# Optimization experiments

Measured on AMD Instinct MI355X. Metric: run time of the kernel, lower is better.

The kernel has to match this reference:

```python
import jax, jax.numpy as jnp
import numpy as np
from jax import lax

D_MODEL = 512
D_INNER = 1024   # expand=2
D_STATE = 16
D_CONV = 4
DT_RANK = 32     # ceil(d_model/16)
D_FFN = 2048
EPS = 1e-6


def _layernorm(x, g, b):
    mu = jnp.mean(x, axis=-1, keepdims=True)
    var = jnp.mean((x - mu) ** 2, axis=-1, keepdims=True)
    return (x - mu) * lax.rsqrt(var + EPS) * g + b


def _mamba(x, in_w, conv_w, conv_b, xproj_w, dt_w, dt_b, A_log, D_vec, out_w):
    # x: [B, L, d_model]
    B, L, _ = x.shape
    xz = jnp.einsum('bld,ed->ble', x, in_w)           # [B, L, 2*d_inner]
    xc, z = xz[..., :D_INNER], xz[..., D_INNER:]
    # causal depthwise conv over time
    xt = xc.transpose(0, 2, 1)                        # [B, d_inner, L]
    kern = conv_w[:, None, :]                         # [d_inner, 1, d_conv]
    xt = lax.conv_general_dilated(xt, kern, (1,), [(D_CONV - 1, 0)],
                                  feature_group_count=D_INNER)
    xc = jax.nn.silu(xt.transpose(0, 2, 1) + conv_b)  # [B, L, d_inner]
    # input-dependent SSM parameters
    x_dbl = jnp.einsum('bld,ed->ble', xc, xproj_w)    # [B, L, dt_rank+2*d_state]
    dt = x_dbl[..., :DT_RANK]
    Bm = x_dbl[..., DT_RANK:DT_RANK + D_STATE]
    Cm = x_dbl[..., DT_RANK + D_STATE:]
    delta = jax.nn.softplus(jnp.einsum('blr,dr->bld', dt, dt_w) + dt_b)  # [B, L, d_inner]
    A = -jnp.exp(A_log)                               # [d_inner, d_state]

    def step(h, inp):
        d_t, u_t, b_t, c_t = inp                      # [B,di],[B,di],[B,ds],[B,ds]
        dA = jnp.exp(d_t[:, :, None] * A)             # [B, di, ds]
        dBu = (d_t * u_t)[:, :, None] * b_t[:, None, :]
        h = dA * h + dBu
        y = jnp.einsum('bds,bs->bd', h, c_t)
        return h, y

    h0 = jnp.zeros((B, D_INNER, D_STATE), x.dtype)
    xs = (delta.transpose(1, 0, 2), xc.transpose(1, 0, 2),
          Bm.transpose(1, 0, 2), Cm.transpose(1, 0, 2))
    _, ys = lax.scan(step, h0, xs)                    # [L, B, d_inner]
    y = ys.transpose(1, 0, 2) + xc * D_vec
    y = y * jax.nn.silu(z)
    return jnp.einsum('ble,de->bld', y, out_w)        # [B, L, d_model]


def setup_inputs() -> dict:
    key = jax.random.key(0)
    ks = iter(jax.random.split(key, 40))
    B, S, T = 8, 512, 1024

    def nrm(shape, scale=0.02):
        return jax.random.normal(next(ks), shape, dtype=jnp.float32) * scale

    def mamba_params(prefix):
        A_log = jnp.log(jnp.broadcast_to(jnp.arange(1, D_STATE + 1, dtype=jnp.float32),
                                         (D_INNER, D_STATE)))
        return {
            prefix + '_in_w': nrm((2 * D_INNER, D_MODEL)),
            prefix + '_conv_w': nrm((D_INNER, D_CONV), 0.1),
            prefix + '_conv_b': jnp.zeros((D_INNER,), jnp.float32),
            prefix + '_xproj_w': nrm((DT_RANK + 2 * D_STATE, D_INNER)),
            prefix + '_dt_w': nrm((D_INNER, DT_RANK), 0.1),
            prefix + '_dt_b': jnp.full((D_INNER,), -4.0, jnp.float32),
            prefix + '_A_log': A_log,
            prefix + '_D_vec': jnp.ones((D_INNER,), jnp.float32),
            prefix + '_out_w': nrm((D_MODEL, D_INNER)),
        }

    inp = {
        'tgt': jax.random.normal(next(ks), (B, S, D_MODEL), dtype=jnp.float32),
        'memory': jax.random.normal(next(ks), (B, T, D_MODEL), dtype=jnp.float32),
    }
    inp.update(mamba_params('self'))
    inp.update(mamba_params('cross'))
    inp.update({
        'ln1_g': jnp.ones((D_MODEL,), jnp.float32), 'ln1_b': jnp.zeros((D_MODEL,), jnp.float32),
        'ln2_g': jnp.ones((D_MODEL,), jnp.float32), 'ln2_b': jnp.zeros((D_MODEL,), jnp.float32),
        'ln3_g': jnp.ones((D_MODEL,), jnp.float32), 'ln3_b': jnp.zeros((D_MODEL,), jnp.float32),
        'ffn_w1': nrm((D_FFN, D_MODEL)), 'ffn_b1': jnp.zeros((D_FFN,), jnp.float32),
        'ffn_w2': nrm((D_MODEL, D_FFN)), 'ffn_b2': jnp.zeros((D_MODEL,), jnp.float32),
    })
    return inp


def reference(tgt, memory,
              self_in_w, self_conv_w, self_conv_b, self_xproj_w, self_dt_w, self_dt_b,
              self_A_log, self_D_vec, self_out_w,
              cross_in_w, cross_conv_w, cross_conv_b, cross_xproj_w, cross_dt_w, cross_dt_b,
              cross_A_log, cross_D_vec, cross_out_w,
              ln1_g, ln1_b, ln2_g, ln2_b, ln3_g, ln3_b,
              ffn_w1, ffn_b1, ffn_w2, ffn_b2):
    S = tgt.shape[1]
    # self-Mamba block (post-norm, dropout=0)
    t2 = _mamba(tgt, self_in_w, self_conv_w, self_conv_b, self_xproj_w,
                self_dt_w, self_dt_b, self_A_log, self_D_vec, self_out_w)
    t = _layernorm(tgt + t2, ln1_g, ln1_b)
    # cross-Mamba: scan over [memory; tgt], keep last S steps
    cat = jnp.concatenate([memory, t], axis=1)
    c2 = _mamba(cat, cross_in_w, cross_conv_w, cross_conv_b, cross_xproj_w,
                cross_dt_w, cross_dt_b, cross_A_log, cross_D_vec, cross_out_w)[:, -S:]
    t = _layernorm(t + c2, ln2_g, ln2_b)
    # positionwise FFN
    f = jnp.einsum('bld,fd->blf', t, ffn_w1) + ffn_b1
    f = jax.nn.relu(f)
    f = jnp.einsum('blf,df->bld', f, ffn_w2) + ffn_b2
    t = _layernorm(t + f, ln3_g, ln3_b)
    return t
```

## Files before the change

kernel.cpp:

```cpp
#include <hip/hip_runtime.h>
#include <math.h>

#define DM    512
#define DI    1024
#define DSN   16
#define DTR   32
#define DFFN  2048
#define BB    8
#define SS    512
#define TTM   1024
#define LCAT  1536
#define CONV_R 8

#define ACT_NONE     0
#define ACT_RELU     1
#define ACT_DELTA    3
#define ACT_XDBL     4

typedef __attribute__((ext_vector_type(8))) short short8;
typedef __attribute__((ext_vector_type(8))) unsigned short ushort8;
typedef __attribute__((ext_vector_type(4))) float f32x4;

#define L2E 1.4426950408889634f

__device__ __forceinline__ unsigned short f2b(float f) {
    unsigned int u = __float_as_uint(f);
    return (unsigned short)((u + 0x7FFFu + ((u >> 16) & 1u)) >> 16);
}
__device__ __forceinline__ float b2f(unsigned short h) {
    return __uint_as_float(((unsigned int)h) << 16);
}
__device__ __forceinline__ float fast_softplus(float v) {
    return (v > 20.f) ? v : __logf(1.f + __expf(v));
}
__device__ __forceinline__ float fexp2(float x) {
#if __has_builtin(__builtin_amdgcn_exp2f)
    return __builtin_amdgcn_exp2f(x);
#else
    float r; asm("v_exp_f32 %0, %1" : "=v"(r) : "v"(x)); return r;
#endif
}
__device__ __forceinline__ float frcp(float x) {
    return __builtin_amdgcn_rcpf(x);
}
__device__ __forceinline__ void gld16(const void* g, void* l) {
    __builtin_amdgcn_global_load_lds(
        (const __attribute__((address_space(1))) void*)g,
        (__attribute__((address_space(3))) void*)l, 16, 0, 0);
}

__device__ __forceinline__ int map_row(int m, int mb, int bs, int ro) {
    int q = m / mb;
    return q * bs + ro + (m - q * mb);
}

__global__ __launch_bounds__(256) void mgemm_kernel(
    const unsigned short* __restrict__ A, int mb, int bs, int ro,
    const unsigned short* __restrict__ W, const float* __restrict__ bias,
    float* __restrict__ Cf, unsigned short* __restrict__ Cb,
    float* __restrict__ C2, float* __restrict__ Cf2,
    int N, int K, int act,
    int omb, int obs, int oro, int ldc, int nofs, int pstr,
    int ysplit, int amb2, int abs2, int aro2, int wofs2,
    int omb2, int obs2, int oro2, int nofs2)
{
    __shared__ __align__(16) unsigned short As[128 * 64];
    __shared__ __align__(16) unsigned short Bs[128 * 64];
    int tid = threadIdx.x;
    int lane = tid & 63, wave = tid >> 6;
    int wy = wave >> 1, wx = wave & 1;
    int bx = blockIdx.x, by = blockIdx.y;
    int nx = gridDim.x, ny = gridDim.y;
    const unsigned short* Wp = W;
    if (ysplit) {
        if (by >= ysplit) {
            by -= ysplit; ny = gridDim.y - ysplit;
            mb = amb2; bs = abs2; ro = aro2; Wp += wofs2;
            omb = omb2; obs = obs2; oro = oro2; nofs = nofs2;
        } else ny = ysplit;
    }
    int f = by * nx + bx;
    int xcd = f & 7, j2 = f >> 3;
    int bandh = ny >> 3;
    int m0 = (xcd * bandh + j2 / nx) * 128;
    int n0 = (j2 % nx) * 128;
    int Kh = K / gridDim.z;
    int kbeg = blockIdx.z * Kh, kend = kbeg + Kh;
    float* Cfo = Cf;
    const float* biaso = bias;
    if (blockIdx.z) { Cfo = Cf2 + (size_t)(blockIdx.z - 1) * pstr; biaso = nullptr; }

    unsigned aoff[4], boff[4];
    unsigned short* la[4];
    unsigned short* lb[4];
    #pragma unroll
    for (int j = 0; j < 4; j++) {
        int c  = wave * 256 + j * 64 + lane;
        int r  = c >> 3;
        int q  = c & 7;
        int g  = q ^ (r & 7);
        int arow = map_row(m0 + r, mb, bs, ro);
        aoff[j] = (unsigned)(arow * K + g * 8);
        boff[j] = (unsigned)((n0 + r) * K + g * 8);
        la[j] = As + (size_t)(wave * 256 + j * 64) * 8;
        lb[j] = Bs + (size_t)(wave * 256 + j * 64) * 8;
    }
    int fm = lane & 15, fg = lane >> 4;
    int sw = fg ^ (fm & 3);
    int b2 = (fm >> 2) & 1;
    const unsigned short* arp = As + ((size_t)(wy * 64 + fm) * 8 + sw) * 8;
    const unsigned short* brp = Bs + ((size_t)(wx * 64 + fm) * 8 + sw) * 8;

    f32x4 acc[4][4];
    #pragma unroll
    for (int i = 0; i < 4; i++)
        #pragma unroll
        for (int j = 0; j < 4; j++) acc[i][j] = 0.f;

    for (int k0 = kbeg; k0 < kend; k0 += 64) {
        #pragma unroll
        for (int j = 0; j < 4; j++) {
            gld16(A  + aoff[j] + k0, la[j]);
            gld16(Wp + boff[j] + k0, lb[j]);
        }
        __syncthreads();
        #pragma unroll
        for (int h = 0; h < 2; h++) {
            int ho = ((h ^ b2) * 32);
            short8 af[4], bfr[4];
            #pragma unroll
            for (int t = 0; t < 4; t++) af[t]  = *(const short8*)(arp + ho + t * 1024);
            #pragma unroll
            for (int t = 0; t < 4; t++) bfr[t] = *(const short8*)(brp + ho + t * 1024);
            #pragma unroll
            for (int i = 0; i < 4; i++)
                #pragma unroll
                for (int j = 0; j < 4; j++)
                    acc[i][j] = __builtin_amdgcn_mfma_f32_16x16x32_bf16(af[i], bfr[j], acc[i][j], 0, 0, 0);
        }
        __syncthreads();
    }

    int en = lane & 15, em = (lane >> 4) * 4;
    if (act == ACT_XDBL) {
        size_t zb = (size_t)blockIdx.z * omb;
        #pragma unroll
        for (int j = 0; j < 4; j++) {
            int n = n0 + wx * 64 + j * 16 + en;
            if (n >= 64) continue;
            #pragma unroll
            for (int i = 0; i < 4; i++) {
                int mbase = m0 + wy * 64 + i * 16 + em;
                #pragma unroll
                for (int r = 0; r < 4; r++)
                    C2[(zb + mbase + r) * 64 + n] = acc[i][j][r];
            }
        }
        return;
    }
    if (act == ACT_DELTA) {
        #pragma unroll
        for (int j = 0; j < 4; j++) {
            int n = n0 + wx * 64 + j * 16 + en;
            float bv = bias[n];
            #pragma unroll
            for (int i = 0; i < 4; i++) {
                int mbase = m0 + wy * 64 + i * 16 + em;
                #pragma unroll
                for (int r = 0; r < 4; r++) {
                    float v = acc[i][j][r] + bv;
                    Cb[(size_t)(mbase + r) * 1024 + n] = f2b(fast_softplus(v));
                }
            }
        }
        return;
    }
    #pragma unroll
    for (int j = 0; j < 4; j++) {
        int n = n0 + wx * 64 + j * 16 + en;
        float bv = biaso ? biaso[n] : 0.f;
        #pragma unroll
        for (int i = 0; i < 4; i++) {
            int mbase = m0 + wy * 64 + i * 16 + em;
            #pragma unroll
            for (int r = 0; r < 4; r++) {
                float v = acc[i][j][r] + bv;
                if (act == ACT_RELU) v = v > 0.f ? v : 0.f;
                int orow = map_row(mbase + r, omb, obs, oro);
                size_t off = (size_t)orow * ldc + nofs + n;
                if (Cb) Cb[off] = f2b(v);
                else    Cfo[off] = v;
            }
        }
    }
}

__global__ __launch_bounds__(256) void xdbl_combine(
    const float* __restrict__ pxd, unsigned short* __restrict__ dtb,
    float* __restrict__ bcout, int M, int Z)
{
    int idx = blockIdx.x * 256 + threadIdx.x;
    int m = idx >> 4, n4 = idx & 15;
    int n = n4 * 4;
    float4 s = make_float4(0.f, 0.f, 0.f, 0.f);
    for (int z = 0; z < Z; z++) {
        float4 p = *(const float4*)(pxd + ((size_t)z * M + m) * 64 + n);
        s.x += p.x; s.y += p.y; s.z += p.z; s.w += p.w;
    }
    if (n < 32) {
        ((ushort4*)(dtb + (size_t)m * 64))[n4] =
            make_ushort4(f2b(s.x), f2b(s.y), f2b(s.z), f2b(s.w));
    } else {
        *(float4*)(bcout + (size_t)m * 32 + (n - 32)) = s;
        ((ushort4*)(dtb + (size_t)m * 64))[n4] = make_ushort4(0, 0, 0, 0);
    }
}

struct PrepPtrs {
    const float* tgt; const float* mem;
    const float* w[6];
    const float* xpj_s; const float* xpj_c;
    const float* dtw_s; const float* dtw_c;
    unsigned short* tgtb; unsigned short* catb; unsigned short* wb;
    unsigned short* xprojb_s; unsigned short* xprojb_c;
    unsigned short* dtwb_s; unsigned short* dtwb_c;
};
__global__ __launch_bounds__(256) void prep_kernel(PrepPtrs p)
{
    int u = blockIdx.x * 256 + threadIdx.x;
    if (u < 524288) {
        float4 v = ((const float4*)p.tgt)[u];
        ((ushort4*)p.tgtb)[u] = make_ushort4(f2b(v.x), f2b(v.y), f2b(v.z), f2b(v.w));
        return;
    }
    if (u < 1572864) {
        int f = u - 524288;
        int b = f >> 17, rem = f & 131071;
        float4 v = ((const float4*)p.mem)[f];
        ((ushort4*)p.catb)[(size_t)b * 196608 + rem] =
            make_ushort4(f2b(v.x), f2b(v.y), f2b(v.z), f2b(v.w));
        return;
    }
    if (u < 2883584) {
        const int cum[7] = {0, 262144, 524288, 655360, 786432, 1048576, 1310720};
        int i = u - 1572864;
        int seg = 0;
        #pragma unroll
        for (int s = 1; s < 6; s++) seg += (i >= cum[s]);
        float4 v = ((const float4*)p.w[seg])[i - cum[seg]];
        ((ushort4*)p.wb)[i] = make_ushort4(f2b(v.x), f2b(v.y), f2b(v.z), f2b(v.w));
        return;
    }
    if (u < 2949120) {
        int i = u - 2883584;
        const float* src = p.xpj_s;
        unsigned short* dst = p.xprojb_s;
        if (i >= 32768) { i -= 32768; src = p.xpj_c; dst = p.xprojb_c; }
        int n = i >> 8;
        ushort4 o = make_ushort4(0, 0, 0, 0);
        if (n < 64) {
            float4 v = ((const float4*)src)[i];
            o = make_ushort4(f2b(v.x), f2b(v.y), f2b(v.z), f2b(v.w));
        }
        ((ushort4*)dst)[i] = o;
        return;
    }
    {
        int i = u - 2949120;
        const float* src = p.dtw_s;
        unsigned short* dst = p.dtwb_s;
        if (i >= 16384) { i -= 16384; src = p.dtw_c; dst = p.dtwb_c; }
        int n = i >> 4, c = (i & 15) * 4;
        ushort4 o = make_ushort4(0, 0, 0, 0);
        if (c < 32) {
            float4 v = *(const float4*)(src + n * 32 + c);
            o = make_ushort4(f2b(v.x), f2b(v.y), f2b(v.z), f2b(v.w));
        }
        ((ushort4*)dst)[i] = o;
    }
}

__global__ __launch_bounds__(256) void conv_silu_kernel(
    const unsigned short* __restrict__ xz,
    const float* __restrict__ cw,
    const float* __restrict__ cb,
    unsigned short* __restrict__ xc, int L, int total)
{
    int idx = blockIdx.x * blockDim.x + threadIdx.x;
    if (idx >= total) return;
    int d8 = idx & 127;
    int d0 = d8 * 8;
    int t  = idx >> 7;
    int nq = L / CONV_R;
    int b  = t / nq;
    int l0 = (t - b * nq) * CONV_R;
    size_t rbase = (size_t)b * L + l0;

    float4 wv[8];
    #pragma unroll
    for (int j = 0; j < 8; j++) wv[j] = *(const float4*)(cw + (d0 + j) * 4);
    float bias[8];
    {
        float4 c0 = ((const float4*)(cb + d0))[0];
        float4 c1 = ((const float4*)(cb + d0))[1];
        bias[0]=c0.x; bias[1]=c0.y; bias[2]=c0.z; bias[3]=c0.w;
        bias[4]=c1.x; bias[5]=c1.y; bias[6]=c1.z; bias[7]=c1.w;
    }
    ushort8 win[CONV_R + 3];
    #pragma unroll
    for (int k = 0; k < 3; k++) {
        ushort8 z;
        #pragma unroll
        for (int j = 0; j < 8; j++) z[j] = 0;
        win[k] = (l0 - 3 + k >= 0)
            ? *(const ushort8*)(xz + (rbase - 3 + k) * 2048 + d0) : z;
    }
    #pragma unroll
    for (int i = 0; i < CONV_R; i++)
        win[3 + i] = *(const ushort8*)(xz + (rbase + i) * 2048 + d0);

    const float* w = (const float*)&wv[0];
    #pragma unroll
    for (int i = 0; i < CONV_R; i++) {
        float acc[8];
        #pragma unroll
        for (int j = 0; j < 8; j++) acc[j] = bias[j];
        #pragma unroll
        for (int k = 0; k < 4; k++) {
            ushort8 v = win[i + k];
            #pragma unroll
            for (int j = 0; j < 8; j++)
                acc[j] = fmaf(b2f(v[j]), w[j * 4 + k], acc[j]);
        }
        ushort8 o;
        #pragma unroll
        for (int j = 0; j < 8; j++)
            o[j] = f2b(acc[j] * frcp(1.f + __expf(-acc[j])));
        *(ushort8*)(xc + (rbase + i) * 1024 + d0) = o;
    }
}

__global__ __launch_bounds__(256) void scan_part1(
    const unsigned short* __restrict__ delta, const unsigned short* __restrict__ xc,
    const float* __restrict__ bc, const float* __restrict__ A_log,
    float* __restrict__ part_h, float* __restrict__ part_s, int L, int CH, int NCr)
{
    __shared__ float bcs[24 * 16];
    int tid = threadIdx.x;
    int dblk = blockIdx.x & 3;
    int rest = blockIdx.x >> 2;
    int c    = rest % NCr;
    int b    = rest / NCr;
    if (c == NCr - 1) return;
    int l0 = c * CH;
    for (int i = tid; i < CH * 16; i += 256) {
        int lr = i >> 4, s = i & 15;
        bcs[i] = bc[((size_t)b * L + l0 + lr) * 32 + s];
    }
    __syncthreads();
    int d    = dblk * 256 + tid;
    float A2[DSN];
    {
        const float4* ap = (const float4*)(A_log + d * DSN);
        #pragma unroll
        for (int q = 0; q < 4; q++) {
            float4 a4 = ap[q];
            A2[q*4+0] = -__expf(a4.x) * L2E;
            A2[q*4+1] = -__expf(a4.y) * L2E;
            A2[q*4+2] = -__expf(a4.z) * L2E;
            A2[q*4+3] = -__expf(a4.w) * L2E;
        }
    }
    float h[DSN];
    #pragma unroll
    for (int s = 0; s < DSN; s++) h[s] = 0.f;
    float ssum = 0.f;
    size_t rb = (size_t)b * L + l0;
    float dl = b2f(delta[rb * DI + d]);
    float u  = b2f(xc[rb * DI + d]);
    for (int i = 0; i < CH; i++) {
        float cdl = dl, cu = u;
        if (i + 1 < CH) {
            size_t rn = rb + i + 1;
            dl = b2f(delta[rn * DI + d]);
            u  = b2f(xc[rn * DI + d]);
        }
        const float* Bm = bcs + i * 16;
        float du = cdl * cu;
        ssum += cdl;
        #pragma unroll
        for (int s = 0; s < DSN; s++)
            h[s] = fmaf(fexp2(cdl * A2[s]), h[s], du * Bm[s]);
    }
    size_t base = ((size_t)(b * NCr + c) * DI + d) * DSN;
    #pragma unroll
    for (int q = 0; q < 4; q++)
        ((float4*)(part_h + base))[q] = make_float4(h[q*4], h[q*4+1], h[q*4+2], h[q*4+3]);
    part_s[(size_t)(b * NCr + c) * DI + d] = ssum;
}

__global__ __launch_bounds__(256) void scan_combine(
    const float* __restrict__ A_log,
    float* __restrict__ part_h, const float* __restrict__ part_s, int NCr)
{
    int idx = blockIdx.x * 256 + threadIdx.x;
    int s  = idx & (DSN - 1);
    int dd = (idx >> 4) & (DI - 1);
    int b  = idx >> 14;
    float A2 = -__expf(A_log[dd * DSN + s]) * L2E;
    float h = 0.f;
    size_t sbase = (size_t)b * NCr * DI + dd;
    size_t hbase = ((size_t)b * NCr * DI + dd) * DSN + s;
    for (int c = 0; c < NCr; c++) {
        float ph = part_h[hbase];
        float S  = part_s[sbase];
        part_h[hbase] = h;
        h = fmaf(fexp2(A2 * S), h, ph);
        hbase += (size_t)DI * DSN;
        sbase += DI;
    }
}

__global__ __launch_bounds__(256) void scan_part2(
    const unsigned short* __restrict__ delta, const unsigned short* __restrict__ xc,
    const float* __restrict__ bc, const unsigned short* __restrict__ xz,
    const float* __restrict__ A_log, const float* __restrict__ Dv,
    const float* __restrict__ part_h,
    unsigned short* __restrict__ out, int L, int CH, int NCr, int c0, int lmin)
{
    __shared__ float bcs[24 * 32];
    int tid = threadIdx.x;
    int dblk = blockIdx.x & 3;
    int rest = blockIdx.x >> 2;
    int ncp  = NCr - c0;
    int c    = c0 + rest % ncp;
    int b    = rest / ncp;
    int l0 = c * CH;
    for (int i = tid; i < CH * 32; i += 256)
        bcs[i] = bc[((size_t)b * L + l0) * 32 + i];
    __syncthreads();
    int d    = dblk * 256 + tid;
    float A2[DSN];
    {
        const float4* ap = (const float4*)(A_log + d * DSN);
        #pragma unroll
        for (int q = 0; q < 4; q++) {
            float4 a4 = ap[q];
            A2[q*4+0] = -__expf(a4.x) * L2E;
            A2[q*4+1] = -__expf(a4.y) * L2E;
            A2[q*4+2] = -__expf(a4.z) * L2E;
            A2[q*4+3] = -__expf(a4.w) * L2E;
        }
    }
    float Dvd = Dv[d];
    size_t base = ((size_t)(b * NCr + c) * DI + d) * DSN;
    float h4[4][4];
    #pragma unroll
    for (int q = 0; q < 4; q++) *((float4*)h4[q]) = ((const float4*)(part_h + base))[q];
    float h[DSN];
    #pragma unroll
    for (int s = 0; s < DSN; s++) h[s] = h4[s >> 2][s & 3];
    size_t rb = (size_t)b * L + l0;
    float dl = b2f(delta[rb * DI + d]);
    float u  = b2f(xc[rb * DI + d]);
    float z  = b2f(xz[rb * 2048 + DI + d]);
    for (int i = 0; i < CH; i++) {
        float cdl = dl, cu = u, cz = z;
        if (i + 1 < CH) {
            size_t rn = rb + i + 1;
            dl = b2f(delta[rn * DI + d]);
            u  = b2f(xc[rn * DI + d]);
            z  = b2f(xz[rn * 2048 + DI + d]);
        }
        const float* Bm = bcs + i * 32;
        const float* Cm = Bm + DSN;
        float du = cdl * cu;
        float y = 0.f;
        #pragma unroll
        for (int s = 0; s < DSN; s++) {
            h[s] = fmaf(fexp2(cdl * A2[s]), h[s], du * Bm[s]);
            y = fmaf(h[s], Cm[s], y);
        }
        if (l0 + i >= lmin) {
            float sil = cz * frcp(1.f + __expf(-cz));
            out[(rb + i) * DI + d] = f2b((y + cu * Dvd) * sil);
        }
    }
}

__global__ __launch_bounds__(128) void addln_kernel(
    const float* __restrict__ a, int amb, int absd, int aro, int lda,
    const float* __restrict__ bsrc, const float* __restrict__ parts, int nparts, int pstr,
    const float* __restrict__ g, const float* __restrict__ be,
    float* __restrict__ outf, int omb, int obsd, int oro, int ldo,
    unsigned short* __restrict__ outb, int bmb, int bbsd, int bro, int ldb)
{
    int m = blockIdx.x, t = threadIdx.x;
    int ar = map_row(m, amb, absd, aro);
    float4 x4 = ((const float4*)(a + (size_t)ar * lda))[t];
    float4 y4 = ((const float4*)(bsrc + (size_t)m * DM))[t];
    float v[4] = {x4.x + y4.x, x4.y + y4.y, x4.z + y4.z, x4.w + y4.w};
    for (int p = 0; p < nparts; p++) {
        float4 z4 = ((const float4*)(parts + (size_t)p * pstr + (size_t)m * DM))[t];
        v[0] += z4.x; v[1] += z4.y; v[2] += z4.z; v[3] += z4.w;
    }
    float sum = v[0] + v[1] + v[2] + v[3];
    float sq  = v[0]*v[0] + v[1]*v[1] + v[2]*v[2] + v[3]*v[3];
    #pragma unroll
    for (int o = 32; o > 0; o >>= 1) {
        sum += __shfl_down(sum, o);
        sq  += __shfl_down(sq, o);
    }
    __shared__ float s0[2], s1[2];
    if ((t & 63) == 0) { s0[t >> 6] = sum; s1[t >> 6] = sq; }
    __syncthreads();
    float tot = s0[0] + s0[1];
    float tsq = s1[0] + s1[1];
    float mu = tot * (1.f / DM);
    float var = tsq * (1.f / DM) - mu * mu;
    float rs = rsqrtf(var + 1e-6f);
    float4 g4 = ((const float4*)g)[t];
    float4 b4 = ((const float4*)be)[t];
    float o0 = (v[0] - mu) * rs * g4.x + b4.x;
    float o1 = (v[1] - mu) * rs * g4.y + b4.y;
    float o2 = (v[2] - mu) * rs * g4.z + b4.z;
    float o3 = (v[3] - mu) * rs * g4.w + b4.w;
    if (outf) {
        int orow = map_row(m, omb, obsd, oro);
        ((float4*)(outf + (size_t)orow * ldo))[t] = make_float4(o0, o1, o2, o3);
    }
    if (outb) {
        int brow = map_row(m, bmb, bbsd, bro);
        ((ushort4*)(outb + (size_t)brow * ldb))[t] =
            make_ushort4(f2b(o0), f2b(o1), f2b(o2), f2b(o3));
    }
}

static void run_scan(const unsigned short* dltb, const unsigned short* xcb, const float* bc,
                     const unsigned short* xzb, const float* A_log, const float* Dv,
                     float* part_h, float* part_s, unsigned short* out, int L, int NCr,
                     int c0, int lmin, hipStream_t stream)
{
    int CH = L / NCr;
    int blocks1 = BB * NCr * (DI / 256);
    scan_part1<<<blocks1, 256, 0, stream>>>(dltb, xcb, bc, A_log, part_h, part_s, L, CH, NCr);
    scan_combine<<<BB * DI * DSN / 256, 256, 0, stream>>>(A_log, part_h, part_s, NCr);
    int blocks2 = BB * (NCr - c0) * (DI / 256);
    scan_part2<<<blocks2, 256, 0, stream>>>(dltb, xcb, bc, xzb, A_log, Dv, part_h, out, L, CH, NCr, c0, lmin);
}

extern "C" void kernel_launch(void* const* d_in, const int* in_sizes, int n_in,
                              void* d_out, int out_size, void* d_ws, size_t ws_size,
                              hipStream_t stream)
{
    const float* tgt       = (const float*)d_in[0];
    const float* memory    = (const float*)d_in[1];
    const float* s_in_w    = (const float*)d_in[2];
    const float* s_conv_w  = (const float*)d_in[3];
    const float* s_conv_b  = (const float*)d_in[4];
    const float* s_xproj_w = (const float*)d_in[5];
    const float* s_dt_w    = (const float*)d_in[6];
    const float* s_dt_b    = (const float*)d_in[7];
    const float* s_A_log   = (const float*)d_in[8];
    const float* s_D_vec   = (const float*)d_in[9];
    const float* s_out_w   = (const float*)d_in[10];
    const float* c_in_w    = (const float*)d_in[11];
    const float* c_conv_w  = (const float*)d_in[12];
    const float* c_conv_b  = (const float*)d_in[13];
    const float* c_xproj_w = (const float*)d_in[14];
    const float* c_dt_w    = (const float*)d_in[15];
    const float* c_dt_b    = (const float*)d_in[16];
    const float* c_A_log   = (const float*)d_in[17];
    const float* c_D_vec   = (const float*)d_in[18];
    const float* c_out_w   = (const float*)d_in[19];
    const float* ln1_g     = (const float*)d_in[20];
    const float* ln1_b     = (const float*)d_in[21];
    const float* ln2_g     = (const float*)d_in[22];
    const float* ln2_b     = (const float*)d_in[23];
    const float* ln3_g     = (const float*)d_in[24];
    const float* ln3_b     = (const float*)d_in[25];
    const float* ffn_w1    = (const float*)d_in[26];
    const float* ffn_b1    = (const float*)d_in[27];
    const float* ffn_w2    = (const float*)d_in[28];
    const float* ffn_b2    = (const float*)d_in[29];
    float* outp = (float*)d_out;

    float* ws     = (float*)d_ws;
    float* bc     = ws;
    float* t1     = bc     + 393216;
    float* tbuf   = t1     + 2097152;
    float* part_h = tbuf   + 2097152;
    float* proj   = part_h;
    float* pparts = part_h + 2097152;
    float* pxd    = part_h;
    float* part_s = part_h + 8388608;
    unsigned short* ub      = (unsigned short*)(part_s + 524288);
    unsigned short* dltb    = ub;
    unsigned short* catb    = dltb    + 12582912;
    unsigned short* tgtb    = catb    + 6291456;
    unsigned short* xzb     = tgtb    + 2097152;
    unsigned short* xcb     = xzb     + 25165824;
    unsigned short* ygb     = xcb     + 12582912;
    unsigned short* tbbf    = ygb     + 12582912;
    unsigned short* s_in_wb = tbbf    + 2097152;
    unsigned short* c_in_wb = s_in_wb + 1048576;
    unsigned short* s_out_wb= c_in_wb + 1048576;
    unsigned short* c_out_wb= s_out_wb+ 524288;
    unsigned short* w1b     = c_out_wb+ 524288;
    unsigned short* w2b     = w1b     + 1048576;
    unsigned short* xprojb_s= w2b     + 1048576;
    unsigned short* xprojb_c= xprojb_s+ 131072;
    unsigned short* dtwb_s  = xprojb_c+ 131072;
    unsigned short* dtwb_c  = dtwb_s  + 65536;
    unsigned short* dtb     = dtwb_c  + 65536;
    unsigned short* fbuf    = xzb;
    float* ffnout  = (float*)dltb;
    float* fparts  = ffnout + 2097152;

    {
        PrepPtrs pp;
        pp.tgt = tgt; pp.mem = memory;
        pp.w[0]=s_in_w; pp.w[1]=c_in_w; pp.w[2]=s_out_w; pp.w[3]=c_out_w; pp.w[4]=ffn_w1; pp.w[5]=ffn_w2;
        pp.xpj_s = s_xproj_w; pp.xpj_c = c_xproj_w;
        pp.dtw_s = s_dt_w;    pp.dtw_c = c_dt_w;
        pp.tgtb = tgtb; pp.catb = catb; pp.wb = s_in_wb;
        pp.xprojb_s = xprojb_s; pp.xprojb_c = xprojb_c;
        pp.dtwb_s = dtwb_s; pp.dtwb_c = dtwb_c;
        prep_kernel<<<11648, 256, 0, stream>>>(pp);
    }

    mgemm_kernel<<<dim3(2048/128, 4096/128), 256, 0, stream>>>(
        tgtb, 4096, 0, 0, s_in_wb, nullptr, nullptr, xzb, nullptr, nullptr, 2048, 512, ACT_NONE,
        4096, 0, 0, 2048, 0, 0,  0, 0,0,0, 0, 0,0,0, 0);
    conv_silu_kernel<<<(BB*(SS/CONV_R)*128 + 255)/256, 256, 0, stream>>>(
        xzb, s_conv_w, s_conv_b, xcb, SS, BB*(SS/CONV_R)*128);
    mgemm_kernel<<<dim3(1, 4096/128, 4), 256, 0, stream>>>(
        xcb, 4096, 0, 0, xprojb_s, nullptr, nullptr, nullptr, pxd, nullptr, 128, 1024, ACT_XDBL,
        4096, 0, 0, 0, 0, 0,  0, 0,0,0, 0, 0,0,0, 0);
    xdbl_combine<<<4096*16/256, 256, 0, stream>>>(pxd, dtb, bc, 4096, 4);
    mgemm_kernel<<<dim3(1024/128, 4096/128), 256, 0, stream>>>(
        dtb, 4096, 0, 0, dtwb_s, s_dt_b, nullptr, dltb, nullptr, nullptr, 1024, 64, ACT_DELTA,
        4096, 0, 0, 1024, 0, 0,  0, 0,0,0, 0, 0,0,0, 0);
    run_scan(dltb, xcb, bc, xzb, s_A_log, s_D_vec, part_h, part_s, ygb, SS, 64, 0, 0, stream);
    mgemm_kernel<<<dim3(512/128, 4096/128, 4), 256, 0, stream>>>(
        ygb, 4096, 0, 0, s_out_wb, nullptr, proj, nullptr, nullptr, pparts, 512, 1024, ACT_NONE,
        4096, 0, 0, 512, 0, 2097152,  0, 0,0,0, 0, 0,0,0, 0);
    addln_kernel<<<4096, 128, 0, stream>>>(
        tgt, 4096, 0, 0, DM, proj, pparts, 3, 2097152, ln1_g, ln1_b,
        t1, 4096, 0, 0, DM, catb, 512, 1536, 1024, DM);

    mgemm_kernel<<<dim3(1024/128, 96 + 32), 256, 0, stream>>>(
        catb, 12288, 0, 0, c_in_wb, nullptr, nullptr, xzb, nullptr, nullptr, 2048, 512, ACT_NONE,
        12288, 0, 0, 2048, 0, 0,
        96, 512, 1536, 1024, 1024 * 512, 512, 1536, 1024, 1024);
    conv_silu_kernel<<<(BB*(LCAT/CONV_R)*128 + 255)/256, 256, 0, stream>>>(
        xzb, c_conv_w, c_conv_b, xcb, LCAT, BB*(LCAT/CONV_R)*128);
    mgemm_kernel<<<dim3(1, 12288/128, 4), 256, 0, stream>>>(
        xcb, 12288, 0, 0, xprojb_c, nullptr, nullptr, nullptr, pxd, nullptr, 128, 1024, ACT_XDBL,
        12288, 0, 0, 0, 0, 0,  0, 0,0,0, 0, 0,0,0, 0);
    xdbl_combine<<<12288*16/256, 256, 0, stream>>>(pxd, dtb, bc, 12288, 4);
    mgemm_kernel<<<dim3(1024/128, 12288/128), 256, 0, stream>>>(
        dtb, 12288, 0, 0, dtwb_c, c_dt_b, nullptr, dltb, nullptr, nullptr, 1024, 64, ACT_DELTA,
        12288, 0, 0, 1024, 0, 0,  0, 0,0,0, 0, 0,0,0, 0);
    run_scan(dltb, xcb, bc, xzb, c_A_log, c_D_vec, part_h, part_s, ygb, LCAT, 64, 42, 1024, stream);
    mgemm_kernel<<<dim3(512/128, 4096/128, 4), 256, 0, stream>>>(
        ygb, 512, 1536, 1024, c_out_wb, nullptr, proj, nullptr, nullptr, pparts, 512, 1024, ACT_NONE,
        4096, 0, 0, 512, 0, 2097152,  0, 0,0,0, 0, 0,0,0, 0);
    addln_kernel<<<4096, 128, 0, stream>>>(
        t1, 4096, 0, 0, DM, proj, pparts, 3, 2097152, ln2_g, ln2_b,
        tbuf, 4096, 0, 0, DM, tbbf, 4096, 0, 0, DM);

    mgemm_kernel<<<dim3(2048/128, 4096/128), 256, 0, stream>>>(
        tbbf, 4096, 0, 0, w1b, ffn_b1, nullptr, fbuf, nullptr, nullptr, 2048, 512, ACT_RELU,
        4096, 0, 0, 2048, 0, 0,  0, 0,0,0, 0, 0,0,0, 0);
    mgemm_kernel<<<dim3(512/128, 4096/128, 4), 256, 0, stream>>>(
        fbuf, 4096, 0, 0, w2b, ffn_b2, ffnout, nullptr, nullptr, fparts, 512, 2048, ACT_NONE,
        4096, 0, 0, 512, 0, 2097152,  0, 0,0,0, 0, 0,0,0, 0);
    addln_kernel<<<4096, 128, 0, stream>>>(
        tbuf, 4096, 0, 0, DM, ffnout, fparts, 3, 2097152, ln3_g, ln3_b,
        outp, 4096, 0, 0, DM, nullptr, 0, 0, 0, 0);
}
```

Baseline: 495.9 us.

## Stage bf16 GEMM epilogue through LDS and batch scan loads with templated chunk size

The GEMM bf16-output epilogue now writes tiles to shared memory and then stores 16-byte vectors per row, replacing scattered 2-byte global stores. ReLU is folded into this path, and the fp32 path is simplified. The scan kernels are templated on chunk length and load each half-chunk of delta/u/z into registers before the recurrence, which exposes more memory-level parallelism than the single-step prefetch. This costs extra LDS, one barrier and more registers.

Measured after the change: 498.3 us. No clear change (+0.5%).

```diff
diff --git a/kernel.cpp b/kernel.cpp
--- a/kernel.cpp
+++ b/kernel.cpp
@@ -64,8 +64,9 @@
     int ysplit, int amb2, int abs2, int aro2, int wofs2,
     int omb2, int obs2, int oro2, int nofs2)
 {
-    __shared__ __align__(16) unsigned short As[128 * 64];
-    __shared__ __align__(16) unsigned short Bs[128 * 64];
+    __shared__ __align__(16) unsigned short smem[128 * 136];
+    unsigned short* As = smem;
+    unsigned short* Bs = smem + 8192;
     int tid = threadIdx.x;
     int lane = tid & 63, wave = tid >> 6;
     int wy = wave >> 1, wx = wave & 1;
@@ -158,20 +159,31 @@
         }
         return;
     }
-    if (act == ACT_DELTA) {
+    if (Cb) {
         #pragma unroll
         for (int j = 0; j < 4; j++) {
-            int n = n0 + wx * 64 + j * 16 + en;
-            float bv = bias[n];
+            int nl = wx * 64 + j * 16 + en;
+            float bv = bias ? bias[n0 + nl] : 0.f;
             #pragma unroll
             for (int i = 0; i < 4; i++) {
-                int mbase = m0 + wy * 64 + i * 16 + em;
+                int ml = wy * 64 + i * 16 + em;
                 #pragma unroll
                 for (int r = 0; r < 4; r++) {
                     float v = acc[i][j][r] + bv;
-                    Cb[(size_t)(mbase + r) * 1024 + n] = f2b(fast_softplus(v));
+                    if (act == ACT_RELU)  v = v > 0.f ? v : 0.f;
+                    if (act == ACT_DELTA) v = fast_softplus(v);
+                    smem[(ml + r) * 136 + nl] = f2b(v);
                 }
             }
+        }
+        __syncthreads();
+        #pragma unroll
+        for (int q = 0; q < 8; q++) {
+            int unit = q * 256 + tid;
+            int row = unit >> 4, c8 = (unit & 15) * 8;
+            ushort8 v = *(const ushort8*)(smem + row * 136 + c8);
+            int orow = map_row(m0 + row, omb, obs, oro);
+            *(ushort8*)(Cb + (size_t)orow * ldc + nofs + n0 + c8) = v;
         }
         return;
     }
@@ -185,11 +197,8 @@
             #pragma unroll
             for (int r = 0; r < 4; r++) {
                 float v = acc[i][j][r] + bv;
-                if (act == ACT_RELU) v = v > 0.f ? v : 0.f;
                 int orow = map_row(mbase + r, omb, obs, oro);
-                size_t off = (size_t)orow * ldc + nofs + n;
-                if (Cb) Cb[off] = f2b(v);
-                else    Cfo[off] = v;
+                Cfo[(size_t)orow * ldc + nofs + n] = v;
             }
         }
     }
@@ -340,12 +349,13 @@
     }
 }
 
+template<int CH>
 __global__ __launch_bounds__(256) void scan_part1(
     const unsigned short* __restrict__ delta, const unsigned short* __restrict__ xc,
     const float* __restrict__ bc, const float* __restrict__ A_log,
-    float* __restrict__ part_h, float* __restrict__ part_s, int L, int CH, int NCr)
-{
-    __shared__ float bcs[24 * 16];
+    float* __restrict__ part_h, float* __restrict__ part_s, int L, int NCr)
+{
+    __shared__ float bcs[CH * 16];
     int tid = threadIdx.x;
     int dblk = blockIdx.x & 3;
     int rest = blockIdx.x >> 2;
@@ -376,21 +386,27 @@
     for (int s = 0; s < DSN; s++) h[s] = 0.f;
     float ssum = 0.f;
     size_t rb = (size_t)b * L + l0;
-    float dl = b2f(delta[rb * DI + d]);
-    float u  = b2f(xc[rb * DI + d]);
-    for (int i = 0; i < CH; i++) {
-        float cdl = dl, cu = u;
-        if (i + 1 < CH) {
-            size_t rn = rb + i + 1;
-            dl = b2f(delta[rn * DI + d]);
-            u  = b2f(xc[rn * DI + d]);
-        }
-        const float* Bm = bcs + i * 16;
-        float du = cdl * cu;
-        ssum += cdl;
-        #pragma unroll
-        for (int s = 0; s < DSN; s++)
-            h[s] = fmaf(fexp2(cdl * A2[s]), h[s], du * Bm[s]);
+    constexpr int HH = CH / 2;
+    #pragma unroll
+    for (int hh = 0; hh < 2; hh++) {
+        unsigned short dls[HH], uss[HH];
+        #pragma unroll
+        for (int i = 0; i < HH; i++) {
+            size_t rn = rb + hh * HH + i;
+            dls[i] = delta[rn * DI + d];
+            uss[i] = xc[rn * DI + d];
+        }
+        #pragma unroll
+        for (int i = 0; i < HH; i++) {
+            int st = hh * HH + i;
+            float cdl = b2f(dls[i]), cu = b2f(uss[i]);
+            const float* Bm = bcs + st * 16;
+            float du = cdl * cu;
+            ssum += cdl;
+            #pragma unroll
+            for (int s = 0; s < DSN; s++)
+                h[s] = fmaf(fexp2(cdl * A2[s]), h[s], du * Bm[s]);
+        }
     }
     size_t base = ((size_t)(b * NCr + c) * DI + d) * DSN;
     #pragma unroll
@@ -421,14 +437,15 @@
     }
 }
 
+template<int CH>
 __global__ __launch_bounds__(256) void scan_part2(
     const unsigned short* __restrict__ delta, const unsigned short* __restrict__ xc,
     const float* __restrict__ bc, const unsigned short* __restrict__ xz,
     const float* __restrict__ A_log, const float* __restrict__ Dv,
     const float* __restrict__ part_h,
-    unsigned short* __restrict__ out, int L, int CH, int NCr, int c0, int lmin)
-{
-    __shared__ float bcs[24 * 32];
+    unsigned short* __restrict__ out, int L, int NCr, int c0, int lmin)
+{
+    __shared__ float bcs[CH * 32];
     int tid = threadIdx.x;
     int dblk = blockIdx.x & 3;
     int rest = blockIdx.x >> 2;
@@ -461,29 +478,35 @@
     #pragma unroll
     for (int s = 0; s < DSN; s++) h[s] = h4[s >> 2][s & 3];
     size_t rb = (size_t)b * L + l0;
-    float dl = b2f(delta[rb * DI + d]);
-    float u  = b2f(xc[rb * DI + d]);
-    float z  = b2f(xz[rb * 2048 + DI + d]);
-    for (int i = 0; i < CH; i++) {
-        float cdl = dl, cu = u, cz = z;
-        if (i + 1 < CH) {
-            size_t rn = rb + i + 1;
-            dl = b2f(delta[rn * DI + d]);
-            u  = b2f(xc[rn * DI + d]);
-            z  = b2f(xz[rn * 2048 + DI + d]);
-        }
-        const float* Bm = bcs + i * 32;
-        const float* Cm = Bm + DSN;
-        float du = cdl * cu;
-        float y = 0.f;
-        #pragma unroll
-        for (int s = 0; s < DSN; s++) {
-            h[s] = fmaf(fexp2(cdl * A2[s]), h[s], du * Bm[s]);
-            y = fmaf(h[s], Cm[s], y);
-        }
-        if (l0 + i >= lmin) {
-            float sil = cz * frcp(1.f + __expf(-cz));
-            out[(rb + i) * DI + d] = f2b((y + cu * Dvd) * sil);
+    constexpr int HH = CH / 2;
+    #pragma unroll
+    for (int hh = 0; hh < 2; hh++) {
+        unsigned short dls[HH], uss[HH], zs[HH];
+        #pragma unroll
+        for (int i = 0; i < HH; i++) {
+            size_t rn = rb + hh * HH + i;
+            dls[i] = delta[rn * DI + d];
+            uss[i] = xc[rn * DI + d];
+            zs[i]  = xz[rn * 2048 + DI + d];
+        }
+        #pragma unroll
+        for (int i = 0; i < HH; i++) {
+            int st = hh * HH + i;
+            float cdl = b2f(dls[i]), cu = b2f(uss[i]);
+            const float* Bm = bcs + st * 32;
+            const float* Cm = Bm + DSN;
+            float du = cdl * cu;
+            float y = 0.f;
+            #pragma unroll
+            for (int s = 0; s < DSN; s++) {
+                h[s] = fmaf(fexp2(cdl * A2[s]), h[s], du * Bm[s]);
+                y = fmaf(h[s], Cm[s], y);
+            }
+            if (l0 + st >= lmin) {
+                float cz = b2f(zs[i]);
+                float sil = cz * frcp(1.f + __expf(-cz));
+                out[(rb + st) * DI + d] = f2b((y + cu * Dvd) * sil);
+            }
         }
     }
 }
@@ -541,12 +564,17 @@
                      float* part_h, float* part_s, unsigned short* out, int L, int NCr,
                      int c0, int lmin, hipStream_t stream)
 {
-    int CH = L / NCr;
     int blocks1 = BB * NCr * (DI / 256);
-    scan_part1<<<blocks1, 256, 0, stream>>>(dltb, xcb, bc, A_log, part_h, part_s, L, CH, NCr);
-    scan_combine<<<BB * DI * DSN / 256, 256, 0, stream>>>(A_log, part_h, part_s, NCr);
     int blocks2 = BB * (NCr - c0) * (DI / 256);
-    scan_part2<<<blocks2, 256, 0, stream>>>(dltb, xcb, bc, xzb, A_log, Dv, part_h, out, L, CH, NCr, c0, lmin);
+    if (L == SS) {
+        scan_part1<8><<<blocks1, 256, 0, stream>>>(dltb, xcb, bc, A_log, part_h, part_s, L, NCr);
+        scan_combine<<<BB * DI * DSN / 256, 256, 0, stream>>>(A_log, part_h, part_s, NCr);
+        scan_part2<8><<<blocks2, 256, 0, stream>>>(dltb, xcb, bc, xzb, A_log, Dv, part_h, out, L, NCr, c0, lmin);
+    } else {
+        scan_part1<24><<<blocks1, 256, 0, stream>>>(dltb, xcb, bc, A_log, part_h, part_s, L, NCr);
+        scan_combine<<<BB * DI * DSN / 256, 256, 0, stream>>>(A_log, part_h, part_s, NCr);
+        scan_part2<24><<<blocks2, 256, 0, stream>>>(dltb, xcb, bc, xzb, A_log, Dv, part_h, out, L, NCr, c0, lmin);
+    }
 }
 
 extern "C" void kernel_launch(void* const* d_in, const int* in_sizes, int n_in,
```
